# Performance work log

Hardware: AMD Instinct MI355X
Metric: run time of the kernel (lower is better)

The kernel has to match this reference:

```python
import jax, jax.numpy as jnp
import numpy as np

HIDDEN = 2048
NUM_HEADS = 8
NUM_KV_HEADS = 2
HEAD_DIM = 256
ROPE_BASE = 1e6
EPS = 1e-6
B, S = 2, 2048


def rms_norm(x, w, eps=EPS):
    # normalize over last dim (head_dim), per-head
    var = jnp.mean(jnp.square(x), axis=-1, keepdims=True)
    return x * jax.lax.rsqrt(var + eps) * w


def rope(x, positions, base=ROPE_BASE):
    # neox-style rotate-half RoPE over full head_dim. x: [B,S,H,D], positions: [B,S]
    d = x.shape[-1]
    inv_freq = 1.0 / (base ** (jnp.arange(0, d, 2, dtype=jnp.float32) / d))
    freqs = positions.astype(jnp.float32)[..., None] * inv_freq  # [B,S,D/2]
    cos = jnp.cos(freqs)[:, :, None, :]
    sin = jnp.sin(freqs)[:, :, None, :]
    x1, x2 = x[..., : d // 2], x[..., d // 2 :]
    return jnp.concatenate([x1 * cos - x2 * sin, x2 * cos + x1 * sin], axis=-1)


def setup_inputs() -> dict:
    key = jax.random.key(0)
    k1, k2, k3 = jax.random.split(key, 3)
    hidden_states = jax.random.normal(k1, (B, S, HIDDEN), dtype=jnp.float32)
    positions = jnp.broadcast_to(jnp.arange(S, dtype=jnp.int32), (B, S))
    qkv_out = (NUM_HEADS + 2 * NUM_KV_HEADS) * HEAD_DIM
    w_qkv = jax.random.normal(k2, (HIDDEN, qkv_out), dtype=jnp.float32) * (HIDDEN ** -0.5)
    w_o = jax.random.normal(k3, (NUM_HEADS * HEAD_DIM, HIDDEN), dtype=jnp.float32) * ((NUM_HEADS * HEAD_DIM) ** -0.5)
    q_norm_w = jnp.ones((HEAD_DIM,), dtype=jnp.float32)
    k_norm_w = jnp.ones((HEAD_DIM,), dtype=jnp.float32)
    return {"hidden_states": hidden_states, "positions": positions, "w_qkv": w_qkv,
            "w_o": w_o, "q_norm_w": q_norm_w, "k_norm_w": k_norm_w}


def reference(hidden_states, positions, w_qkv, w_o, q_norm_w, k_norm_w):
    b, s, _ = hidden_states.shape
    q_size = NUM_HEADS * HEAD_DIM
    kv_size = NUM_KV_HEADS * HEAD_DIM
    qkv = hidden_states @ w_qkv  # [B,S,q+2kv]
    q, k, v = jnp.split(qkv, [q_size, q_size + kv_size], axis=-1)
    q = q.reshape(b, s, NUM_HEADS, HEAD_DIM)
    k = k.reshape(b, s, NUM_KV_HEADS, HEAD_DIM)
    v = v.reshape(b, s, NUM_KV_HEADS, HEAD_DIM)
    # per-head RMSNorm; v_norm has no learned scale (weight fixed to ones)
    q = rms_norm(q, q_norm_w)
    k = rms_norm(k, k_norm_w)
    v = rms_norm(v, jnp.ones((HEAD_DIM,), dtype=v.dtype))
    # RoPE
    q = rope(q, positions)
    k = rope(k, positions)
    # GQA: repeat kv heads
    g = NUM_HEADS // NUM_KV_HEADS
    k = jnp.repeat(k, g, axis=2)
    v = jnp.repeat(v, g, axis=2)
    # causal attention with scaling = 1.0 (as in module)
    scores = jnp.einsum("bqhd,bkhd->bhqk", q, k)
    mask = jnp.tril(jnp.ones((s, s), dtype=bool))
    scores = jnp.where(mask, scores, jnp.finfo(scores.dtype).min)
    probs = jax.nn.softmax(scores, axis=-1)
    attn = jnp.einsum("bhqk,bkhd->bqhd", probs, v).reshape(b, s, NUM_HEADS * HEAD_DIM)
    return attn @ w_o
```

## Files before the change

### kernel.cpp

```cpp
#include <hip/hip_runtime.h>


#define HID  2048
#define NH   8
#define NKV  2
#define HD   256
#define SB   2048
#define BB   2
#define MTOK (BB * SB)
#define NQKV ((NH + 2 * NKV) * HD)

typedef _Float16  f16x8 __attribute__((ext_vector_type(8)));
typedef float     f32x4 __attribute__((ext_vector_type(4)));

__device__ __forceinline__ unsigned short f2h(float f) {
  _Float16 h = (_Float16)f;
  return __builtin_bit_cast(unsigned short, h);
}

__device__ __forceinline__ void async_copy16(const unsigned short* g, unsigned short* l) {
  __builtin_amdgcn_global_load_lds(
      (const __attribute__((address_space(1))) unsigned int*)g,
      (__attribute__((address_space(3))) unsigned int*)l, 16, 0, 0);
}

__device__ __forceinline__ int swz4(int r) { return (r + (r >> 2)) & 3; }

template <int OUT_MODE, int BN>
__global__ __launch_bounds__(512, 2) void gemm_p2(const unsigned short* __restrict__ A,
                                                  const unsigned short* __restrict__ Bt,
                                                  void* __restrict__ Cg,
                                                  int M, int N, int K) {
  constexpr int WN  = BN / 4;
  constexpr int NF  = BN / 64;
  constexpr int LPTB = BN / 128;
  __shared__ __align__(16) unsigned short Ash[4 * 256 * 32];
  __shared__ __align__(16) unsigned short Bsh[4 * BN * 32];

  const int t = threadIdx.x;
  const int lane = t & 63, w = t >> 6;
  const int quad = lane >> 4, m15 = lane & 15;
  const int wm = w >> 2, wn = w & 3;

  const int nwg = gridDim.x * gridDim.y;
  int bid = blockIdx.y * gridDim.x + blockIdx.x;
  if ((nwg & 7) == 0) bid = (bid & 7) * (nwg >> 3) + (bid >> 3);
  const int bx = bid % gridDim.x, by = bid / gridDim.x;
  const int m0 = by * 256, n0 = bx * BN;

  const unsigned short* aSrc[2];
  int aDst[2];
#pragma unroll
  for (int j = 0; j < 2; ++j) {
    const int c = t + j * 512;
    const int row = c >> 2, slot = c & 3;
    aSrc[j] = A + (size_t)(m0 + row) * K + ((slot ^ swz4(row)) * 8);
    aDst[j] = c * 8;
  }
  const unsigned short* bSrc[LPTB];
  int bDst[LPTB];
#pragma unroll
  for (int j = 0; j < LPTB; ++j) {
    const int c = t + j * 512;
    const int row = c >> 2, slot = c & 3;
    bSrc[j] = Bt + (size_t)(n0 + row) * K + ((slot ^ swz4(row)) * 8);
    bDst[j] = c * 8;
  }

  int offA[8], offB[NF];
#pragma unroll
  for (int i = 0; i < 8; ++i) {
    const int ra = wm * 128 + i * 16 + m15;
    offA[i] = ra * 32 + ((quad ^ swz4(ra)) * 8);
  }
#pragma unroll
  for (int j = 0; j < NF; ++j) {
    const int rb = wn * WN + j * 16 + m15;
    offB[j] = rb * 32 + ((quad ^ swz4(rb)) * 8);
  }

  const f32x4 vz = {0.f, 0.f, 0.f, 0.f};
  f32x4 acc[8][NF];
#pragma unroll
  for (int i = 0; i < 8; ++i)
#pragma unroll
    for (int j = 0; j < NF; ++j) acc[i][j] = vz;

  const int NK = K >> 5;

  for (int pt = 0; pt < 3; ++pt) {
    const int kb = pt * 32;
    unsigned short* ab = &Ash[pt * 8192];
    unsigned short* bb = &Bsh[pt * (BN * 32)];
#pragma unroll
    for (int j = 0; j < 2; ++j) async_copy16(aSrc[j] + kb, ab + aDst[j]);
#pragma unroll
    for (int j = 0; j < LPTB; ++j) async_copy16(bSrc[j] + kb, bb + bDst[j]);
  }
  if constexpr (BN == 256) asm volatile("s_waitcnt vmcnt(8)" ::: "memory");
  else                     asm volatile("s_waitcnt vmcnt(6)" ::: "memory");
  __builtin_amdgcn_s_barrier();

  for (int kt = 0; kt < NK; ++kt) {
    const int buf = kt & 3;
    const unsigned short* Ab = &Ash[buf * 8192];
    const unsigned short* Bb = &Bsh[buf * (BN * 32)];
    const int s3 = kt + 3;
    const int kb3 = s3 * 32;
    unsigned short* a3 = &Ash[(s3 & 3) * 8192];
    unsigned short* b3 = &Bsh[(s3 & 3) * (BN * 32)];
    const bool stage3 = (s3 < NK);

    f16x8 af[4], bf[NF];
#pragma unroll
    for (int i = 0; i < 4; ++i) af[i] = *(const f16x8*)&Ab[offA[i]];
#pragma unroll
    for (int j = 0; j < NF; ++j) bf[j] = *(const f16x8*)&Bb[offB[j]];
    if (stage3) {
#pragma unroll
      for (int j = 0; j < 2; ++j) async_copy16(aSrc[j] + kb3, a3 + aDst[j]);
    }
    __builtin_amdgcn_s_barrier();
    asm volatile("s_waitcnt lgkmcnt(0)" ::: "memory");
    __builtin_amdgcn_sched_barrier(0);
    __builtin_amdgcn_s_setprio(1);
#pragma unroll
    for (int i = 0; i < 4; ++i)
#pragma unroll
      for (int j = 0; j < NF; ++j)
        acc[i][j] = __builtin_amdgcn_mfma_f32_16x16x32_f16(af[i], bf[j], acc[i][j], 0, 0, 0);
    __builtin_amdgcn_s_setprio(0);
    __builtin_amdgcn_s_barrier();

    f16x8 ag[4];
#pragma unroll
    for (int i = 0; i < 4; ++i) ag[i] = *(const f16x8*)&Ab[offA[4 + i]];
    if (stage3) {
#pragma unroll
      for (int j = 0; j < LPTB; ++j) async_copy16(bSrc[j] + kb3, b3 + bDst[j]);
    }
    __builtin_amdgcn_s_barrier();
    asm volatile("s_waitcnt lgkmcnt(0)" ::: "memory");
    __builtin_amdgcn_sched_barrier(0);
    __builtin_amdgcn_s_setprio(1);
#pragma unroll
    for (int i = 0; i < 4; ++i)
#pragma unroll
      for (int j = 0; j < NF; ++j)
        acc[4 + i][j] = __builtin_amdgcn_mfma_f32_16x16x32_f16(ag[i], bf[j], acc[4 + i][j], 0, 0, 0);
    __builtin_amdgcn_s_setprio(0);
    if (stage3) {
      if constexpr (BN == 256) asm volatile("s_waitcnt vmcnt(8)" ::: "memory");
      else                     asm volatile("s_waitcnt vmcnt(6)" ::: "memory");
    } else {
      asm volatile("s_waitcnt vmcnt(0)" ::: "memory");
    }
    __builtin_amdgcn_s_barrier();
  }

#pragma unroll
  for (int i = 0; i < 8; ++i)
#pragma unroll
    for (int j = 0; j < NF; ++j)
#pragma unroll
      for (int r = 0; r < 4; ++r) {
        const int gm = m0 + wm * 128 + i * 16 + quad * 4 + r;
        const int gn = n0 + wn * WN + j * 16 + m15;
        const float v = acc[i][j][r];
        if (OUT_MODE == 2) ((float*)Cg)[(size_t)gm * N + gn] = v;
        else               ((unsigned short*)Cg)[(size_t)gm * N + gn] = f2h(v);
      }
}

__global__ __launch_bounds__(256) void cvt_f32_f16(const float* __restrict__ in,
                                                   unsigned short* __restrict__ out, int n4) {
  const int i = blockIdx.x * 256 + threadIdx.x;
  if (i >= n4) return;
  const float4 v = ((const float4*)in)[i];
  ushort4 o = {f2h(v.x), f2h(v.y), f2h(v.z), f2h(v.w)};
  ((ushort4*)out)[i] = o;
}

__global__ __launch_bounds__(256) void transpose_f2h(const float* __restrict__ in,
                                                     unsigned short* __restrict__ out,
                                                     int R, int C) {
  __shared__ float tile[64 * 68];
  const int r0 = blockIdx.y * 64, c0 = blockIdx.x * 64;
  const int t = threadIdx.x;
#pragma unroll
  for (int p = 0; p < 4; ++p) {
    const int idx = t + p * 256;
    const int rr = idx >> 4, cc = (idx & 15) * 4;
    *(float4*)&tile[rr * 68 + cc] = *(const float4*)&in[(size_t)(r0 + rr) * C + c0 + cc];
  }
  __syncthreads();
#pragma unroll
  for (int p = 0; p < 2; ++p) {
    const int idx = t + p * 256;
    const int dr = idx >> 3, sc = (idx & 7) * 8;
    union { uint4 v; unsigned short s[8]; } o;
#pragma unroll
    for (int e = 0; e < 8; ++e) o.s[e] = f2h(tile[(sc + e) * 68 + dr]);
    *(uint4*)&out[(size_t)(c0 + dr) * R + r0 + sc] = o.v;
  }
}

__global__ __launch_bounds__(256) void normrope(const unsigned short* __restrict__ qkv,
                                                const int* __restrict__ pos,
                                                const float* __restrict__ qw,
                                                const float* __restrict__ kw,
                                                unsigned short* __restrict__ Qh,
                                                unsigned short* __restrict__ Kh,
                                                unsigned short* __restrict__ Vh) {
  const int tok = blockIdx.x;
  const int b = tok >> 11, s = tok & 2047;
  const int t = threadIdx.x, w = t >> 6, lane = t & 63;
  const float p = (float)pos[tok];
  const int dbase = lane * 4;
  const int s5 = s & 31;
  const int sp = (s & ~31) | (((s5 >> 2) & 3) << 3) | (((s5 >> 4) & 1) << 2) | (s5 & 3);

  for (int it = 0; it < 3; ++it) {
    const int slot = it * 4 + w;
    const unsigned short* src = qkv + (size_t)tok * NQKV + slot * 256 + dbase;
    union { uint2 u; _Float16 h[4]; } rd;
    rd.u = *(const uint2*)src;
    float y[4];
#pragma unroll
    for (int e = 0; e < 4; ++e) y[e] = (float)rd.h[e];
    float ssq = y[0] * y[0] + y[1] * y[1] + y[2] * y[2] + y[3] * y[3];
#pragma unroll
    for (int off = 1; off < 64; off <<= 1) ssq += __shfl_xor(ssq, off);
    const float rn = rsqrtf(ssq * (1.f / 256.f) + 1e-6f);

    if (slot < 8) {
#pragma unroll
      for (int e = 0; e < 4; ++e) y[e] *= rn * qw[dbase + e];
    } else if (slot < 10) {
#pragma unroll
      for (int e = 0; e < 4; ++e) y[e] *= rn * kw[dbase + e];
    } else {
#pragma unroll
      for (int e = 0; e < 4; ++e) y[e] *= rn;
    }

    unsigned short* dst;
    if (slot < 8)       dst = Qh + ((size_t)(b * NH + slot) * SB + s) * HD + dbase;
    else if (slot < 10) dst = Kh + ((size_t)(b * NKV + slot - 8) * SB + s) * HD + dbase;
    else                dst = Vh + ((size_t)(b * NKV + slot - 10) * SB + sp) * HD + dbase;

    float outv[4];
    if (slot < 10) {
      const int i0 = dbase & 127;
      const bool lo = (lane < 32);
#pragma unroll
      for (int e = 0; e < 4; ++e) {
        const float partner = __shfl_xor(y[e], 32);
        const float invf = expf(-(float)(i0 + e) * 0.10793368f);
        const float fr = p * invf;
        const float cv = cosf(fr), sv = sinf(fr);
        outv[e] = lo ? (y[e] * cv - partner * sv) : (y[e] * cv + partner * sv);
      }
    } else {
#pragma unroll
      for (int e = 0; e < 4; ++e) outv[e] = y[e];
    }
    union { uint2 u; _Float16 h[4]; } wr;
#pragma unroll
    for (int e = 0; e < 4; ++e) wr.h[e] = (_Float16)outv[e];
    *(uint2*)dst = wr.u;
  }
}

__global__ __launch_bounds__(256) void transpose_u16(const unsigned short* __restrict__ in,
                                                     unsigned short* __restrict__ out,
                                                     int R, int C, size_t ibs, size_t obs) {
  __shared__ unsigned short tile[64 * 72];
  const unsigned short* ib = in + blockIdx.z * ibs;
  unsigned short* ob = out + blockIdx.z * obs;
  const int r0 = blockIdx.y * 64, c0 = blockIdx.x * 64;
  const int t = threadIdx.x;
#pragma unroll
  for (int pck = 0; pck < 2; ++pck) {
    const int c = t + pck * 256;
    const int rr = c >> 3, cc = (c & 7) * 8;
    *(uint4*)&tile[rr * 72 + cc] = *(const uint4*)&ib[(size_t)(r0 + rr) * C + c0 + cc];
  }
  __syncthreads();
#pragma unroll
  for (int pck = 0; pck < 2; ++pck) {
    const int c = t + pck * 256;
    const int dr = c >> 3, sc = (c & 7) * 8;
    union { uint4 v; unsigned short s[8]; } o;
#pragma unroll
    for (int e = 0; e < 8; ++e) o.s[e] = tile[(sc + e) * 72 + dr];
    *(uint4*)&ob[(size_t)(c0 + dr) * R + r0 + sc] = o.v;
  }
}

__global__ __launch_bounds__(512, 2) void flash_attn(const unsigned short* __restrict__ Qh,
                                                     const unsigned short* __restrict__ Kh,
                                                     const unsigned short* __restrict__ Vt,
                                                     unsigned short* __restrict__ attn) {
  __shared__ __align__(16) unsigned char SMEM[132096];
  unsigned short* Ksh = (unsigned short*)SMEM;
  unsigned short* Vsh = (unsigned short*)(SMEM + 65536);
  float*         MLx  = (float*)(SMEM + 131072);
  float*         mergeO = (float*)SMEM;

  const int pairi = blockIdx.x;
  const int h = blockIdx.y, b = blockIdx.z;
  const int kv = h >> 2;
  const int t = threadIdx.x, w = t >> 6, lane = t & 63;
  const int wq = w & 3, team = w >> 2;
  const int quad = lane >> 4, m15 = lane & 15;

  const unsigned short* Kb = Kh + (size_t)(b * NKV + kv) * SB * HD;
  const unsigned short* Vb = Vt + (size_t)(b * NKV + kv) * HD * SB;

  const int krow = t >> 5, kchunk = t & 31;
  const int vrow = t >> 3, vchunk = t & 7;

  const f32x4 vz = {0.f, 0.f, 0.f, 0.f};

  for (int jb = 0; jb < 2; ++jb) {
    const int qt = jb ? (31 - pairi) : pairi;
    const int q0 = qt * 64, qw0 = q0 + wq * 16;
    const int qlane = qw0 + m15;

    f16x8 aq[8];
    const unsigned short* qb = Qh + ((size_t)(b * NH + h) * SB + qw0 + m15) * HD + quad * 8;
#pragma unroll
    for (int ks = 0; ks < 8; ++ks) aq[ks] = *(const f16x8*)(qb + ks * 32);

    f32x4 o[16];
#pragma unroll
    for (int i = 0; i < 16; ++i) o[i] = vz;
    float mrow = -1e30f, lrow = 0.f;

    const int nkt = (q0 + 64) >> 6;

#pragma unroll
    for (int shot = 0; shot < 4; ++shot) {
      const int r = krow + 16 * shot;
      async_copy16(Kb + (size_t)r * HD + ((kchunk ^ (r & 7)) * 8),
                   &Ksh[4096 * shot + t * 8]);
    }
#pragma unroll
    for (int shot = 0; shot < 4; ++shot) {
      const int d = vrow + 64 * shot;
      async_copy16(Vb + (size_t)d * SB + ((vchunk ^ (d & 7)) * 8),
                   &Vsh[4096 * shot + t * 8]);
    }
    __syncthreads();

    for (int kt = 0; kt < nkt; ++kt) {
      const int k0 = kt * 64;
      const int par = kt & 1;

      if (kt + 1 < nkt) {
        const int kn = k0 + 64;
        const int pn = par ^ 1;
#pragma unroll
        for (int shot = 0; shot < 4; ++shot) {
          const int r = krow + 16 * shot;
          async_copy16(Kb + (size_t)(kn + r) * HD + ((kchunk ^ (r & 7)) * 8),
                       &Ksh[pn * 16384 + 4096 * shot + t * 8]);
        }
#pragma unroll
        for (int shot = 0; shot < 4; ++shot) {
          const int d = vrow + 64 * shot;
          async_copy16(Vb + (size_t)d * SB + kn + ((vchunk ^ (d & 7)) * 8),
                       &Vsh[pn * 16384 + 4096 * shot + t * 8]);
        }
      }

      const unsigned short* KB = &Ksh[par * 16384];
      const unsigned short* VB = &Vsh[par * 16384];

      f32x4 sv[2];
      sv[0] = vz; sv[1] = vz;
#pragma unroll
      for (int g = 0; g < 2; ++g) {
        const int key = team * 32 + g * 16 + m15;
        const unsigned short* kr = &KB[key * 256];
        const int sw = (key & 7);
#pragma unroll
        for (int ks = 0; ks < 8; ++ks) {
          const f16x8 ak = *(const f16x8*)&kr[((4 * ks + quad) ^ sw) * 8];
          sv[g] = __builtin_amdgcn_mfma_f32_16x16x32_f16(ak, aq[ks], sv[g], 0, 0, 0);
        }
      }

      const bool last = (kt == nkt - 1);
      float p2[2][4];
#pragma unroll
      for (int g = 0; g < 2; ++g)
#pragma unroll
        for (int r = 0; r < 4; ++r) {
          float s = sv[g][r];
          if (last && (k0 + team * 32 + g * 16 + quad * 4 + r) > qlane) s = -3.0e38f;
          p2[g][r] = s;
        }
      float tm = fmaxf(fmaxf(fmaxf(p2[0][0], p2[0][1]), fmaxf(p2[0][2], p2[0][3])),
                       fmaxf(fmaxf(p2[1][0], p2[1][1]), fmaxf(p2[1][2], p2[1][3])));
      tm = fmaxf(tm, __shfl_xor(tm, 16));
      tm = fmaxf(tm, __shfl_xor(tm, 32));
      if (!__all(tm <= mrow)) {
        const float mnew = fmaxf(mrow, tm);
        const float alpha = __expf(mrow - mnew);
        lrow *= alpha;
#pragma unroll
        for (int dbi = 0; dbi < 16; ++dbi) o[dbi] *= alpha;
        mrow = mnew;
      }
      float rs = 0.f;
#pragma unroll
      for (int g = 0; g < 2; ++g)
#pragma unroll
        for (int r = 0; r < 4; ++r) { p2[g][r] = __expf(p2[g][r] - mrow); rs += p2[g][r]; }
      rs += __shfl_xor(rs, 16);
      rs += __shfl_xor(rs, 32);
      lrow += rs;

      f16x8 bp;
#pragma unroll
      for (int g = 0; g < 2; ++g)
#pragma unroll
        for (int r = 0; r < 4; ++r) bp[g * 4 + r] = (_Float16)p2[g][r];

#pragma unroll
      for (int dbi = 0; dbi < 16; ++dbi) {
        const int d = dbi * 16 + m15;
        const f16x8 av = *(const f16x8*)&VB[d * 64 + (((team * 4 + quad) ^ (d & 7)) * 8)];
        o[dbi] = __builtin_amdgcn_mfma_f32_16x16x32_f16(av, bp, o[dbi], 0, 0, 0);
      }

      __syncthreads();
    }

    if (quad == 0) {
      MLx[w * 32 + m15 * 2]     = mrow;
      MLx[w * 32 + m15 * 2 + 1] = lrow;
    }
    {
      float* mo = mergeO + w * 2176;
#pragma unroll
      for (int ii = 0; ii < 8; ++ii) {
        const int dbi = team ? ii : (8 + ii);
#pragma unroll
        for (int r = 0; r < 4; ++r)
          mo[(ii * 16 + quad * 4 + r) * 17 + m15] = o[dbi][r];
      }
    }
    __syncthreads();
    {
      const int pw = w ^ 4;
      const float* pmo = mergeO + pw * 2176;
      const float pm = MLx[pw * 32 + m15 * 2];
      const float pl = MLx[pw * 32 + m15 * 2 + 1];
      const float mm = fmaxf(mrow, pm);
      const float a0 = __expf(mrow - mm);
      const float a1 = __expf(pm - mm);
      const float invl = 1.0f / (a0 * lrow + a1 * pl);
      const int q = qlane;
#pragma unroll
      for (int ii = 0; ii < 8; ++ii) {
        const int dbi = team ? (8 + ii) : ii;
        union { uint2 u; _Float16 hh[4]; } st;
#pragma unroll
        for (int r = 0; r < 4; ++r) {
          const float po = pmo[(ii * 16 + quad * 4 + r) * 17 + m15];
          st.hh[r] = (_Float16)((a0 * o[dbi][r] + a1 * po) * invl);
        }
        const int dcol = team * 128 + ii * 16 + quad * 4;
        *(uint2*)&attn[(size_t)(b * SB + q) * (NH * HD) + h * HD + dcol] = st.u;
      }
    }
    __syncthreads();
  }
}

static constexpr size_t OFF_HB   = 0;
static constexpr size_t OFF_QH   = 0;
static constexpr size_t OFF_W1T  = 16777216;
static constexpr size_t OFF_KH   = 16777216;
static constexpr size_t OFF_VH   = 20971520;
static constexpr size_t OFF_VT   = 25165824;
static constexpr size_t OFF_WOT  = 29360128;
static constexpr size_t OFF_QKV  = 37748736;
static constexpr size_t OFF_ATTN = OFF_QKV;

extern "C" void kernel_launch(void* const* d_in, const int* in_sizes, int n_in,
                              void* d_out, int out_size, void* d_ws, size_t ws_size,
                              hipStream_t stream) {
  const float* hidden    = (const float*)d_in[0];
  const int*   positions = (const int*)d_in[1];
  const float* w_qkv     = (const float*)d_in[2];
  const float* w_o       = (const float*)d_in[3];
  const float* qw        = (const float*)d_in[4];
  const float* kw        = (const float*)d_in[5];
  float* out = (float*)d_out;
  char* ws = (char*)d_ws;

  unsigned short* hb    = (unsigned short*)(ws + OFF_HB);
  unsigned short* wqkvT = (unsigned short*)(ws + OFF_W1T);
  unsigned short* woT   = (unsigned short*)(ws + OFF_WOT);
  unsigned short* qkvb  = (unsigned short*)(ws + OFF_QKV);
  unsigned short* attnb = (unsigned short*)(ws + OFF_ATTN);
  unsigned short* Qhb   = (unsigned short*)(ws + OFF_QH);
  unsigned short* Khb   = (unsigned short*)(ws + OFF_KH);
  unsigned short* Vhb   = (unsigned short*)(ws + OFF_VH);
  unsigned short* Vtb   = (unsigned short*)(ws + OFF_VT);

  cvt_f32_f16<<<dim3((MTOK * HID / 4 + 255) / 256), 256, 0, stream>>>(hidden, hb, MTOK * HID / 4);
  transpose_f2h<<<dim3(NQKV / 64, HID / 64), 256, 0, stream>>>(w_qkv, wqkvT, HID, NQKV);
  transpose_f2h<<<dim3(HID / 64, HID / 64), 256, 0, stream>>>(w_o, woT, HID, HID);

  gemm_p2<0, 256><<<dim3(NQKV / 256, MTOK / 256), 512, 0, stream>>>(hb, wqkvT, qkvb, MTOK, NQKV, HID);

  normrope<<<dim3(MTOK), 256, 0, stream>>>(qkvb, positions, qw, kw, Qhb, Khb, Vhb);

  transpose_u16<<<dim3(HD / 64, SB / 64, BB * NKV), 256, 0, stream>>>(Vhb, Vtb, SB, HD,
                                                                     (size_t)SB * HD, (size_t)SB * HD);

  flash_attn<<<dim3(16, NH, BB), 512, 0, stream>>>(Qhb, Khb, Vtb, attnb);

  gemm_p2<2, 128><<<dim3(HID / 128, MTOK / 256), 512, 0, stream>>>(attnb, woT, out, MTOK, HID, HID);
}
```

Measured before the change: 337.7 us.

## Fuse QK norm, RoPE and V transpose into QKV GEMM epilogue; merge prep kernels

```diff
diff --git a/kernel.cpp b/kernel.cpp
--- a/kernel.cpp
+++ b/kernel.cpp
@@ -26,16 +26,23 @@
 
 __device__ __forceinline__ int swz4(int r) { return (r + (r >> 2)) & 3; }
 
-template <int OUT_MODE, int BN>
+template <int MODE, int BN>
 __global__ __launch_bounds__(512, 2) void gemm_p2(const unsigned short* __restrict__ A,
                                                   const unsigned short* __restrict__ Bt,
                                                   void* __restrict__ Cg,
-                                                  int M, int N, int K) {
+                                                  int M, int N, int K,
+                                                  const int* __restrict__ pos,
+                                                  const float* __restrict__ qw,
+                                                  const float* __restrict__ kw,
+                                                  unsigned short* __restrict__ Qh,
+                                                  unsigned short* __restrict__ Kh,
+                                                  unsigned short* __restrict__ Vt) {
   constexpr int WN  = BN / 4;
   constexpr int NF  = BN / 64;
   constexpr int LPTB = BN / 128;
-  __shared__ __align__(16) unsigned short Ash[4 * 256 * 32];
-  __shared__ __align__(16) unsigned short Bsh[4 * BN * 32];
+  __shared__ __align__(16) unsigned short SMG[4 * 256 * 32 + 4 * BN * 32];
+  unsigned short* Ash = SMG;
+  unsigned short* Bsh = SMG + 4 * 256 * 32;
 
   const int t = threadIdx.x;
   const int lane = t & 63, w = t >> 6;
@@ -158,35 +165,140 @@
     __builtin_amdgcn_s_barrier();
   }
 
-#pragma unroll
-  for (int i = 0; i < 8; ++i)
-#pragma unroll
-    for (int j = 0; j < NF; ++j)
-#pragma unroll
-      for (int r = 0; r < 4; ++r) {
-        const int gm = m0 + wm * 128 + i * 16 + quad * 4 + r;
-        const int gn = n0 + wn * WN + j * 16 + m15;
-        const float v = acc[i][j][r];
-        if (OUT_MODE == 2) ((float*)Cg)[(size_t)gm * N + gn] = v;
-        else               ((unsigned short*)Cg)[(size_t)gm * N + gn] = f2h(v);
-      }
+  if constexpr (MODE == 2) {
+#pragma unroll
+    for (int i = 0; i < 8; ++i)
+#pragma unroll
+      for (int j = 0; j < NF; ++j)
+#pragma unroll
+        for (int r = 0; r < 4; ++r) {
+          const int gm = m0 + wm * 128 + i * 16 + quad * 4 + r;
+          const int gn = n0 + wn * WN + j * 16 + m15;
+          ((float*)Cg)[(size_t)gm * N + gn] = acc[i][j][r];
+        }
+  } else {
+    const int st = (bx < 8) ? 0 : (bx < 10 ? 1 : 2);
+    constexpr int ES = 260;
+    float invf[4];
+    if (st < 2) {
+#pragma unroll
+      for (int e = 0; e < 4; ++e)
+        invf[e] = __expf(-(float)(((lane * 4) & 127) + e) * 0.10793368f);
+    }
+    const bool lo = (lane < 32);
+
+    for (int half = 0; half < 2; ++half) {
+      if (wm == half) {
+#pragma unroll
+        for (int i = 0; i < 8; ++i)
+#pragma unroll
+          for (int j = 0; j < NF; ++j)
+#pragma unroll
+            for (int r = 0; r < 4; ++r)
+              SMG[(i * 16 + quad * 4 + r) * ES + wn * 64 + j * 16 + m15] = f2h(acc[i][j][r]);
+      }
+      __syncthreads();
+
+#pragma unroll
+      for (int ti = 0; ti < 16; ++ti) {
+        const int tl = w * 16 + ti;
+        const int gtok = m0 + half * 128 + tl;
+        const int b = gtok >> 11, s = gtok & 2047;
+        union { uint2 u; _Float16 h[4]; } rd;
+        rd.u = *(const uint2*)&SMG[tl * ES + lane * 4];
+        float y[4];
+#pragma unroll
+        for (int e = 0; e < 4; ++e) y[e] = (float)rd.h[e];
+        float ssq = y[0] * y[0] + y[1] * y[1] + y[2] * y[2] + y[3] * y[3];
+#pragma unroll
+        for (int off = 1; off < 64; off <<= 1) ssq += __shfl_xor(ssq, off);
+        const float rn = rsqrtf(ssq * (1.f / 256.f) + 1e-6f);
+
+        if (st == 0) {
+#pragma unroll
+          for (int e = 0; e < 4; ++e) y[e] *= rn * qw[lane * 4 + e];
+        } else if (st == 1) {
+#pragma unroll
+          for (int e = 0; e < 4; ++e) y[e] *= rn * kw[lane * 4 + e];
+        } else {
+#pragma unroll
+          for (int e = 0; e < 4; ++e) y[e] *= rn;
+        }
+
+        union { uint2 u; _Float16 h[4]; } wr;
+        if (st < 2) {
+          const float p = (float)pos[gtok];
+#pragma unroll
+          for (int e = 0; e < 4; ++e) {
+            const float partner = __shfl_xor(y[e], 32);
+            const float fr = p * invf[e];
+            const float cv = cosf(fr), sv = sinf(fr);
+            wr.h[e] = (_Float16)(lo ? (y[e] * cv - partner * sv)
+                                    : (y[e] * cv + partner * sv));
+          }
+          unsigned short* dst = (st == 0)
+              ? Qh + ((size_t)(b * NH + bx) * SB + s) * HD + lane * 4
+              : Kh + ((size_t)(b * NKV + (bx - 8)) * SB + s) * HD + lane * 4;
+          *(uint2*)dst = wr.u;
+        } else {
+#pragma unroll
+          for (int e = 0; e < 4; ++e) wr.h[e] = (_Float16)y[e];
+          *(uint2*)&SMG[tl * ES + lane * 4] = wr.u;
+        }
+      }
+
+      if (st == 2) {
+        __syncthreads();
+        const int kv = bx - 10;
+#pragma unroll
+        for (int rep = 0; rep < 32; ++rep) {
+          const int d = w + 8 * rep;
+          const int tp = lane * 2;
+          const unsigned short vlo = SMG[tp * ES + d];
+          const unsigned short vhi = SMG[(tp + 1) * ES + d];
+          const int gs = m0 + half * 128 + tp;
+          const int b = gs >> 11, s = gs & 2047;
+          const int s5 = s & 31;
+          const int sp = (s & ~31) | (((s5 >> 2) & 3) << 3) | (((s5 >> 4) & 1) << 2) | (s5 & 3);
+          *(unsigned int*)&Vt[((size_t)(b * NKV + kv) * HD + d) * SB + sp] =
+              (unsigned)vlo | ((unsigned)vhi << 16);
+        }
+      }
+      __syncthreads();
+    }
+  }
 }
 
-__global__ __launch_bounds__(256) void cvt_f32_f16(const float* __restrict__ in,
-                                                   unsigned short* __restrict__ out, int n4) {
-  const int i = blockIdx.x * 256 + threadIdx.x;
-  if (i >= n4) return;
-  const float4 v = ((const float4*)in)[i];
-  ushort4 o = {f2h(v.x), f2h(v.y), f2h(v.z), f2h(v.w)};
-  ((ushort4*)out)[i] = o;
-}
-
-__global__ __launch_bounds__(256) void transpose_f2h(const float* __restrict__ in,
-                                                     unsigned short* __restrict__ out,
-                                                     int R, int C) {
+__global__ __launch_bounds__(256) void prep(const float* __restrict__ hidden,
+                                            unsigned short* __restrict__ hb,
+                                            const float* __restrict__ w_qkv,
+                                            unsigned short* __restrict__ wqkvT,
+                                            const float* __restrict__ w_o,
+                                            unsigned short* __restrict__ woT) {
   __shared__ float tile[64 * 68];
-  const int r0 = blockIdx.y * 64, c0 = blockIdx.x * 64;
+  const int bid = blockIdx.x;
   const int t = threadIdx.x;
+
+  if (bid < 8192) {
+    const int i = bid * 256 + t;
+    const float4 v = ((const float4*)hidden)[i];
+    ushort4 o = {f2h(v.x), f2h(v.y), f2h(v.z), f2h(v.w)};
+    ((ushort4*)hb)[i] = o;
+    return;
+  }
+
+  const float* in;
+  unsigned short* out;
+  int R, C, r0, c0;
+  if (bid < 9728) {
+    const int bb = bid - 8192;
+    in = w_qkv; out = wqkvT; R = HID; C = NQKV;
+    r0 = (bb / 48) * 64; c0 = (bb % 48) * 64;
+  } else {
+    const int bb = bid - 9728;
+    in = w_o; out = woT; R = HID; C = HID;
+    r0 = (bb / 32) * 64; c0 = (bb % 32) * 64;
+  }
 #pragma unroll
   for (int p = 0; p < 4; ++p) {
     const int idx = t + p * 256;
@@ -202,99 +314,6 @@
 #pragma unroll
     for (int e = 0; e < 8; ++e) o.s[e] = f2h(tile[(sc + e) * 68 + dr]);
     *(uint4*)&out[(size_t)(c0 + dr) * R + r0 + sc] = o.v;
-  }
-}
-
-__global__ __launch_bounds__(256) void normrope(const unsigned short* __restrict__ qkv,
-                                                const int* __restrict__ pos,
-                                                const float* __restrict__ qw,
-                                                const float* __restrict__ kw,
-                                                unsigned short* __restrict__ Qh,
-                                                unsigned short* __restrict__ Kh,
-                                                unsigned short* __restrict__ Vh) {
-  const int tok = blockIdx.x;
-  const int b = tok >> 11, s = tok & 2047;
-  const int t = threadIdx.x, w = t >> 6, lane = t & 63;
-  const float p = (float)pos[tok];
-  const int dbase = lane * 4;
-  const int s5 = s & 31;
-  const int sp = (s & ~31) | (((s5 >> 2) & 3) << 3) | (((s5 >> 4) & 1) << 2) | (s5 & 3);
-
-  for (int it = 0; it < 3; ++it) {
-    const int slot = it * 4 + w;
-    const unsigned short* src = qkv + (size_t)tok * NQKV + slot * 256 + dbase;
-    union { uint2 u; _Float16 h[4]; } rd;
-    rd.u = *(const uint2*)src;
-    float y[4];
-#pragma unroll
-    for (int e = 0; e < 4; ++e) y[e] = (float)rd.h[e];
-    float ssq = y[0] * y[0] + y[1] * y[1] + y[2] * y[2] + y[3] * y[3];
-#pragma unroll
-    for (int off = 1; off < 64; off <<= 1) ssq += __shfl_xor(ssq, off);
-    const float rn = rsqrtf(ssq * (1.f / 256.f) + 1e-6f);
-
-    if (slot < 8) {
-#pragma unroll
-      for (int e = 0; e < 4; ++e) y[e] *= rn * qw[dbase + e];
-    } else if (slot < 10) {
-#pragma unroll
-      for (int e = 0; e < 4; ++e) y[e] *= rn * kw[dbase + e];
-    } else {
-#pragma unroll
-      for (int e = 0; e < 4; ++e) y[e] *= rn;
-    }
-
-    unsigned short* dst;
-    if (slot < 8)       dst = Qh + ((size_t)(b * NH + slot) * SB + s) * HD + dbase;
-    else if (slot < 10) dst = Kh + ((size_t)(b * NKV + slot - 8) * SB + s) * HD + dbase;
-    else                dst = Vh + ((size_t)(b * NKV + slot - 10) * SB + sp) * HD + dbase;
-
-    float outv[4];
-    if (slot < 10) {
-      const int i0 = dbase & 127;
-      const bool lo = (lane < 32);
-#pragma unroll
-      for (int e = 0; e < 4; ++e) {
-        const float partner = __shfl_xor(y[e], 32);
-        const float invf = expf(-(float)(i0 + e) * 0.10793368f);
-        const float fr = p * invf;
-        const float cv = cosf(fr), sv = sinf(fr);
-        outv[e] = lo ? (y[e] * cv - partner * sv) : (y[e] * cv + partner * sv);
-      }
-    } else {
-#pragma unroll
-      for (int e = 0; e < 4; ++e) outv[e] = y[e];
-    }
-    union { uint2 u; _Float16 h[4]; } wr;
-#pragma unroll
-    for (int e = 0; e < 4; ++e) wr.h[e] = (_Float16)outv[e];
-    *(uint2*)dst = wr.u;
-  }
-}
-
-__global__ __launch_bounds__(256) void transpose_u16(const unsigned short* __restrict__ in,
-                                                     unsigned short* __restrict__ out,
-                                                     int R, int C, size_t ibs, size_t obs) {
-  __shared__ unsigned short tile[64 * 72];
-  const unsigned short* ib = in + blockIdx.z * ibs;
-  unsigned short* ob = out + blockIdx.z * obs;
-  const int r0 = blockIdx.y * 64, c0 = blockIdx.x * 64;
-  const int t = threadIdx.x;
-#pragma unroll
-  for (int pck = 0; pck < 2; ++pck) {
-    const int c = t + pck * 256;
-    const int rr = c >> 3, cc = (c & 7) * 8;
-    *(uint4*)&tile[rr * 72 + cc] = *(const uint4*)&ib[(size_t)(r0 + rr) * C + c0 + cc];
-  }
-  __syncthreads();
-#pragma unroll
-  for (int pck = 0; pck < 2; ++pck) {
-    const int c = t + pck * 256;
-    const int dr = c >> 3, sc = (c & 7) * 8;
-    union { uint4 v; unsigned short s[8]; } o;
-#pragma unroll
-    for (int e = 0; e < 8; ++e) o.s[e] = tile[(sc + e) * 72 + dr];
-    *(uint4*)&ob[(size_t)(c0 + dr) * R + r0 + sc] = o.v;
   }
 }
 
@@ -481,15 +500,13 @@
   }
 }
 
-static constexpr size_t OFF_HB   = 0;
 static constexpr size_t OFF_QH   = 0;
-static constexpr size_t OFF_W1T  = 16777216;
 static constexpr size_t OFF_KH   = 16777216;
-static constexpr size_t OFF_VH   = 20971520;
-static constexpr size_t OFF_VT   = 25165824;
-static constexpr size_t OFF_WOT  = 29360128;
-static constexpr size_t OFF_QKV  = 37748736;
-static constexpr size_t OFF_ATTN = OFF_QKV;
+static constexpr size_t OFF_VT   = 20971520;
+static constexpr size_t OFF_W1T  = 25165824;
+static constexpr size_t OFF_WOT  = 37748736;
+static constexpr size_t OFF_HB   = 46137344;
+static constexpr size_t OFF_ATTN = OFF_HB;
 
 extern "C" void kernel_launch(void* const* d_in, const int* in_sizes, int n_in,
                               void* d_out, int out_size, void* d_ws, size_t ws_size,
@@ -506,25 +523,18 @@
   unsigned short* hb    = (unsigned short*)(ws + OFF_HB);
   unsigned short* wqkvT = (unsigned short*)(ws + OFF_W1T);
   unsigned short* woT   = (unsigned short*)(ws + OFF_WOT);
-  unsigned short* qkvb  = (unsigned short*)(ws + OFF_QKV);
   unsigned short* attnb = (unsigned short*)(ws + OFF_ATTN);
   unsigned short* Qhb   = (unsigned short*)(ws + OFF_QH);
   unsigned short* Khb   = (unsigned short*)(ws + OFF_KH);
-  unsigned short* Vhb   = (unsigned short*)(ws + OFF_VH);
   unsigned short* Vtb   = (unsigned short*)(ws + OFF_VT);
 
-  cvt_f32_f16<<<dim3((MTOK * HID / 4 + 255) / 256), 256, 0, stream>>>(hidden, hb, MTOK * HID / 4);
-  transpose_f2h<<<dim3(NQKV / 64, HID / 64), 256, 0, stream>>>(w_qkv, wqkvT, HID, NQKV);
-  transpose_f2h<<<dim3(HID / 64, HID / 64), 256, 0, stream>>>(w_o, woT, HID, HID);
-
-  gemm_p2<0, 256><<<dim3(NQKV / 256, MTOK / 256), 512, 0, stream>>>(hb, wqkvT, qkvb, MTOK, NQKV, HID);
-
-  normrope<<<dim3(MTOK), 256, 0, stream>>>(qkvb, positions, qw, kw, Qhb, Khb, Vhb);
-
-  transpose_u16<<<dim3(HD / 64, SB / 64, BB * NKV), 256, 0, stream>>>(Vhb, Vtb, SB, HD,
-                                                                     (size_t)SB * HD, (size_t)SB * HD);
+  prep<<<dim3(10752), 256, 0, stream>>>(hidden, hb, w_qkv, wqkvT, w_o, woT);
+
+  gemm_p2<3, 256><<<dim3(NQKV / 256, MTOK / 256), 512, 0, stream>>>(
+      hb, wqkvT, nullptr, MTOK, NQKV, HID, positions, qw, kw, Qhb, Khb, Vtb);
 
   flash_attn<<<dim3(16, NH, BB), 512, 0, stream>>>(Qhb, Khb, Vtb, attnb);
 
-  gemm_p2<2, 128><<<dim3(HID / 128, MTOK / 256), 512, 0, stream>>>(attnb, woT, out, MTOK, HID, HID);
+  gemm_p2<2, 128><<<dim3(HID / 128, MTOK / 256), 512, 0, stream>>>(
+      attnb, woT, out, MTOK, HID, HID, nullptr, nullptr, nullptr, nullptr, nullptr, nullptr);
 }
```

Result: no change. 332.1 us (-1.7%).
